# Performance work log

Measured on AMD Instinct MI355X. Metric: run time of the kernel, lower is better.

Reference implementation:

```python
import jax, jax.numpy as jnp
import numpy as np

B, T, H, NH, V = 2, 2048, 512, 8, 32000
HD = H // NH  # head dim

def setup_inputs() -> dict:
    key = jax.random.key(0)
    ks = jax.random.split(key, 15)
    s = 0.02
    rn = lambda k, shp: (jax.random.normal(k, shp, dtype=jnp.float32) * s)
    return {
        "ixs": jax.random.randint(ks[0], (B, T), 0, V, dtype=jnp.int32),
        "tok_emb": rn(ks[1], (V, H)),
        "pos_emb": rn(ks[2], (1, T, H)),
        "W_prj": rn(ks[3], (H, H)),
        "Wq": rn(ks[4], (H, H)), "bq": rn(ks[5], (H,)),
        "Wk": rn(ks[6], (H, H)), "bk": rn(ks[7], (H,)),
        "Wv": rn(ks[8], (H, H)), "bv": rn(ks[9], (H,)),
        "W1": rn(ks[10], (H, H)), "b1": rn(ks[11], (H,)),
        "W2": rn(ks[12], (V, H)), "b2": rn(ks[13], (V,)),
    }

def reference(ixs, tok_emb, pos_emb, W_prj, Wq, bq, Wk, bk, Wv, bv, W1, b1, W2, b2):
    b, t = ixs.shape
    # embeddings + projection (prj1 has no bias)
    x = tok_emb[ixs] + pos_emb[:, :t, :]          # [B,T,H]
    x = x @ W_prj.T                                # [B,T,H]
    # multi-head causal attention; NOTE: scale uses full hidden dim (allH**0.5)
    def heads(W, bias):
        return (x @ W.T + bias).reshape(b, t, NH, HD).transpose(0, 2, 1, 3)  # [B,nH,T,HD]
    q, k, v = heads(Wq, bq), heads(Wk, bk), heads(Wv, bv)
    att = jnp.einsum('bhqd,bhkd->bhqk', q, k) / (H ** 0.5)  # [B,nH,T,T]
    causal = jnp.tril(jnp.ones((t, t), dtype=bool))
    att = jnp.where(causal, att, -jnp.inf)
    w = jax.nn.softmax(att, axis=-1)
    y = jnp.einsum('bhqk,bhkd->bhqd', w, v)        # [B,nH,T,HD]
    y = y.transpose(0, 2, 1, 3).reshape(b, t, H)   # [B,T,H]
    # MLP: Linear->ReLU->Linear->ReLU (final ReLU per original loop condition)
    h1 = jax.nn.relu(y @ W1.T + b1)                # [B,T,H]
    out = jax.nn.relu(h1 @ W2.T + b2)              # [B,T,V]
    return out
```

## Files before the change

kernel.cpp:

```cpp
#include <hip/hip_runtime.h>
#include <stdint.h>
#include <stddef.h>

#define TSEQ   2048
#define HDIM   512
#define NHEADS 8
#define HEADD  64
#define NVOCAB 32000
#define NROWS  4096

typedef unsigned short ushort_t;
typedef __bf16 bf16x8 __attribute__((ext_vector_type(8)));
typedef float  f32x4  __attribute__((ext_vector_type(4)));
typedef unsigned short us8 __attribute__((ext_vector_type(8)));
typedef unsigned short us4 __attribute__((ext_vector_type(4)));
typedef unsigned short us2 __attribute__((ext_vector_type(2)));

__device__ __forceinline__ ushort_t f2bf(float f){
  union { float f; unsigned int u; } v; v.f = f;
  unsigned int u = v.u;
  u += 0x7FFFu + ((u >> 16) & 1u);
  return (ushort_t)(u >> 16);
}

__device__ __forceinline__ void gload_lds16(const ushort_t* g, ushort_t* l){
  __builtin_amdgcn_global_load_lds(
      (const __attribute__((address_space(1))) void*)g,
      (__attribute__((address_space(3))) void*)l, 16, 0, 0);
}

#define CVT_N4   4423680
#define CVT_TOT  4424064
__global__ void cvt_all_kernel(const float* __restrict__ Wprj, const float* __restrict__ Wq,
                               const float* __restrict__ Wk,   const float* __restrict__ Wv,
                               const float* __restrict__ W1,   const float* __restrict__ W2,
                               const float* __restrict__ bq,   const float* __restrict__ bk,
                               const float* __restrict__ bv,
                               ushort_t* __restrict__ wdst, float* __restrict__ bqkv){
  int stride = gridDim.x * blockDim.x;
  for (int i = blockIdx.x * blockDim.x + threadIdx.x; i < CVT_TOT; i += stride){
    if (i < CVT_N4){
      const float* src; int j;
      if (i < 327680){
        int w = i >> 16;
        j = i & 65535;
        src = (w == 0) ? Wprj : (w == 1) ? Wq : (w == 2) ? Wk : (w == 3) ? Wv : W1;
      } else {
        j = i - 327680;
        src = W2;
      }
      float4 f = ((const float4*)src)[j];
      us4 o;
      o[0] = f2bf(f.x); o[1] = f2bf(f.y); o[2] = f2bf(f.z); o[3] = f2bf(f.w);
      ((us4*)wdst)[i] = o;
    } else {
      int j = i - CVT_N4;
      const float* src = (j < 128) ? bq : (j < 256) ? bk : bv;
      int jj = j & 127;
      ((float4*)bqkv)[j] = ((const float4*)src)[jj];
    }
  }
}

__global__ void embed_kernel(const int* __restrict__ ixs, const float* __restrict__ tok,
                             const float* __restrict__ pos, ushort_t* __restrict__ x0){
  const int r = blockIdx.x;
  const int t = r & (TSEQ - 1);
  const int ix = ixs[r];
  const int j = threadIdx.x;
  const float2 a = ((const float2*)(tok + (size_t)ix * HDIM))[j];
  const float2 p = ((const float2*)(pos + (size_t)t * HDIM))[j];
  us2 o; o[0] = f2bf(a.x + p.x); o[1] = f2bf(a.y + p.y);
  *(us2*)(x0 + (size_t)r * HDIM + j * 2) = o;
}

template<int HAS_BIAS, int RELU, int OUT_F32>
__global__ __launch_bounds__(256) void gemm2_kernel(
    const ushort_t* __restrict__ A, const ushort_t* __restrict__ W,
    const float* __restrict__ bias, void* __restrict__ outp,
    int M, int N, int K)
{
  __shared__ ushort_t As[2][128 * 64];
  __shared__ ushort_t Bs[2][128 * 64];
  const int tid  = threadIdx.x;
  const int wave = tid >> 6;
  const int lane = tid & 63;
  const int lr   = lane & 15;
  const int lg   = lane >> 4;
  const int wr   = wave >> 1, wc = wave & 1;

  const int nwg = gridDim.x;
  const int cpx = nwg >> 3;
  const int g   = (blockIdx.x & 7) * cpx + (blockIdx.x >> 3);
  const int nby = M >> 7;
  const int by  = g % nby;
  const int bx  = g / nby;
  const int row0 = by << 7;
  const int col0 = bx << 7;

  f32x4 acc[4][4];
#pragma unroll
  for (int m = 0; m < 4; m++)
#pragma unroll
    for (int n = 0; n < 4; n++) acc[m][n] = (f32x4){0.f, 0.f, 0.f, 0.f};

  const int e    = tid * 8;
  const int srow = e >> 6;
  const int gch  = (((e & 63) >> 3) ^ (srow & 7)) * 8;
  const ushort_t* gA = A + (size_t)(row0 + srow) * K + gch;
  const ushort_t* gB = W + (size_t)(col0 + srow) * K + gch;
  const int ldsoff = wave * 512;

#pragma unroll
  for (int p = 0; p < 4; p++){
    gload_lds16(gA + (size_t)(p * 32) * K, &As[0][p * 2048 + ldsoff]);
    gload_lds16(gB + (size_t)(p * 32) * K, &Bs[0][p * 2048 + ldsoff]);
  }
  __syncthreads();

  const int NT = K >> 6;
  for (int t = 0; t < NT; ++t){
    const int cur = t & 1;
    if (t + 1 < NT){
      const int ko = (t + 1) << 6;
#pragma unroll
      for (int p = 0; p < 4; p++){
        gload_lds16(gA + (size_t)(p * 32) * K + ko, &As[cur ^ 1][p * 2048 + ldsoff]);
        gload_lds16(gB + (size_t)(p * 32) * K + ko, &Bs[cur ^ 1][p * 2048 + ldsoff]);
      }
    }
#pragma unroll
    for (int kk = 0; kk < 64; kk += 32){
      const int rch = (((kk >> 3) + lg) ^ (lr & 7)) * 8;
      bf16x8 af[4], bfr[4];
#pragma unroll
      for (int m = 0; m < 4; m++)
        af[m] = __builtin_bit_cast(bf16x8,
            *(const us8*)&As[cur][(wr * 64 + m * 16 + lr) * 64 + rch]);
#pragma unroll
      for (int n = 0; n < 4; n++)
        bfr[n] = __builtin_bit_cast(bf16x8,
            *(const us8*)&Bs[cur][(wc * 64 + n * 16 + lr) * 64 + rch]);
#pragma unroll
      for (int m = 0; m < 4; m++)
#pragma unroll
        for (int n = 0; n < 4; n++)
          acc[m][n] = __builtin_amdgcn_mfma_f32_16x16x32_bf16(bfr[n], af[m], acc[m][n], 0, 0, 0);
    }
    __syncthreads();
  }

#pragma unroll
  for (int n = 0; n < 4; n++){
    const int colb = col0 + wc * 64 + n * 16 + lg * 4;
    f32x4 b4 = (f32x4){0.f, 0.f, 0.f, 0.f};
    if (HAS_BIAS) b4 = *(const f32x4*)&bias[colb];
#pragma unroll
    for (int m = 0; m < 4; m++){
      const int row = row0 + wr * 64 + m * 16 + lr;
      float v0 = acc[m][n][0] + b4[0], v1 = acc[m][n][1] + b4[1];
      float v2 = acc[m][n][2] + b4[2], v3 = acc[m][n][3] + b4[3];
      if (RELU){ v0 = fmaxf(v0,0.f); v1 = fmaxf(v1,0.f); v2 = fmaxf(v2,0.f); v3 = fmaxf(v3,0.f); }
      if (OUT_F32){
        f32x4 o = {v0, v1, v2, v3};
        *(f32x4*)&((float*)outp)[(size_t)row * N + colb] = o;
      } else {
        us4 o; o[0] = f2bf(v0); o[1] = f2bf(v1); o[2] = f2bf(v2); o[3] = f2bf(v3);
        *(us4*)&((ushort_t*)outp)[(size_t)row * N + colb] = o;
      }
    }
  }
}

#define NKT 16
__global__ __launch_bounds__(512, 2) void gemm_big_kernel(
    const ushort_t* __restrict__ A, const ushort_t* __restrict__ W,
    const float* __restrict__ bias, float* __restrict__ outp)
{
  __shared__ ushort_t Asb[3][256 * 32];
  __shared__ ushort_t Bsb[3][256 * 32];
  const int K = HDIM, N = NVOCAB;
  const int tid  = threadIdx.x;
  const int wave = tid >> 6;
  const int lane = tid & 63;
  const int lr   = lane & 15;
  const int lg   = lane >> 4;
  const int wr   = wave >> 2;
  const int wc   = wave & 3;
  const int tt   = (blockIdx.x & 7) * 250 + (blockIdx.x >> 3);
  const int bx   = tt >> 4;
  const int by   = tt & 15;
  const int row0 = by << 8;
  const int col0 = bx << 8;

  const int rA   = tid >> 2;
  const int csw  = ((tid & 3) ^ (rA & 3) ^ ((rA >> 2) & 3)) * 8;
  const int swzc = (lg ^ (lr & 3) ^ ((lr >> 2) & 3)) * 8;

  f32x4 acc[8][4];
#pragma unroll
  for (int m = 0; m < 8; m++)
#pragma unroll
    for (int n = 0; n < 4; n++) acc[m][n] = (f32x4){0.f, 0.f, 0.f, 0.f};

  {
    const ushort_t* gA = A + (size_t)(row0 + rA) * K + csw;
    const ushort_t* gW = W + (size_t)(col0 + rA) * K + csw;
#pragma unroll
    for (int t = 0; t < 2; t++){
      gload_lds16(gA + t * 32,                       &Asb[t][wave * 512]);
      gload_lds16(gA + (size_t)128 * K + t * 32,     &Asb[t][4096 + wave * 512]);
      gload_lds16(gW + t * 32,                       &Bsb[t][wave * 512]);
      gload_lds16(gW + (size_t)128 * K + t * 32,     &Bsb[t][4096 + wave * 512]);
    }
  }
  asm volatile("s_waitcnt vmcnt(4)" ::: "memory");
  __builtin_amdgcn_s_barrier();

  for (int t = 0; t < NKT; ++t){
    const ushort_t* Ac = &Asb[t % 3][0];
    const ushort_t* Bc = &Bsb[t % 3][0];
    ushort_t* An = &Asb[(t + 2) % 3][0];
    ushort_t* Bn = &Bsb[(t + 2) % 3][0];
    const bool pf = (t + 2 < NKT);
    const int kg = (t + 2) * 32;

    bf16x8 bfr[4], af[4];
#pragma unroll
    for (int n = 0; n < 4; n++)
      bfr[n] = __builtin_bit_cast(bf16x8,
          *(const us8*)&Bc[(wc * 64 + n * 16 + lr) * 32 + swzc]);
#pragma unroll
    for (int q = 0; q < 4; q++)
      af[q] = __builtin_bit_cast(bf16x8,
          *(const us8*)&Ac[(wr * 128 + q * 16 + lr) * 32 + swzc]);
    if (pf){
      gload_lds16(A + (size_t)(row0 + rA) * K + kg + csw,       An + wave * 512);
      gload_lds16(A + (size_t)(row0 + rA + 128) * K + kg + csw, An + 4096 + wave * 512);
    }
    __builtin_amdgcn_s_barrier();
    asm volatile("s_waitcnt lgkmcnt(0)" ::: "memory");
    __builtin_amdgcn_sched_barrier(0);
    __builtin_amdgcn_s_setprio(1);
#pragma unroll
    for (int q = 0; q < 4; q++)
#pragma unroll
      for (int n = 0; n < 4; n++)
        acc[q][n] = __builtin_amdgcn_mfma_f32_16x16x32_bf16(bfr[n], af[q], acc[q][n], 0, 0, 0);
    __builtin_amdgcn_s_setprio(0);
    __builtin_amdgcn_sched_barrier(0);
    __builtin_amdgcn_s_barrier();

#pragma unroll
    for (int q = 0; q < 4; q++)
      af[q] = __builtin_bit_cast(bf16x8,
          *(const us8*)&Ac[(wr * 128 + (q + 4) * 16 + lr) * 32 + swzc]);
    if (pf){
      gload_lds16(W + (size_t)(col0 + rA) * K + kg + csw,       Bn + wave * 512);
      gload_lds16(W + (size_t)(col0 + rA + 128) * K + kg + csw, Bn + 4096 + wave * 512);
    }
    __builtin_amdgcn_s_barrier();
    asm volatile("s_waitcnt lgkmcnt(0)" ::: "memory");
    __builtin_amdgcn_sched_barrier(0);
    __builtin_amdgcn_s_setprio(1);
#pragma unroll
    for (int q = 0; q < 4; q++)
#pragma unroll
      for (int n = 0; n < 4; n++)
        acc[q + 4][n] = __builtin_amdgcn_mfma_f32_16x16x32_bf16(bfr[n], af[q], acc[q + 4][n], 0, 0, 0);
    __builtin_amdgcn_s_setprio(0);
    __builtin_amdgcn_sched_barrier(0);
    if (t < NKT - 2) { asm volatile("s_waitcnt vmcnt(4)" ::: "memory"); }
    else             { asm volatile("s_waitcnt vmcnt(0)" ::: "memory"); }
    __builtin_amdgcn_s_barrier();
  }

#pragma unroll
  for (int n = 0; n < 4; n++){
    const int colb = col0 + wc * 64 + n * 16 + lg * 4;
    const f32x4 b4 = *(const f32x4*)&bias[colb];
#pragma unroll
    for (int m = 0; m < 8; m++){
      const int row = row0 + wr * 128 + m * 16 + lr;
      f32x4 o;
      o[0] = fmaxf(acc[m][n][0] + b4[0], 0.f);
      o[1] = fmaxf(acc[m][n][1] + b4[1], 0.f);
      o[2] = fmaxf(acc[m][n][2] + b4[2], 0.f);
      o[3] = fmaxf(acc[m][n][3] + b4[3], 0.f);
      __builtin_nontemporal_store(o, (f32x4*)&outp[(size_t)row * N + colb]);
    }
  }
}

__global__ __launch_bounds__(256) void attn_kernel(
    const ushort_t* __restrict__ qkv, ushort_t* __restrict__ y)
{
  __shared__ ushort_t Ks[64 * 64];
  __shared__ ushort_t Vt[64 * 64];
  __shared__ ushort_t Ps[4][16 * 64];
  const int qt   = 31 - blockIdx.x;
  const int hb   = blockIdx.y;
  const int b    = hb >> 3;
  const int h    = hb & 7;
  const int tid  = threadIdx.x;
  const int wave = tid >> 6, lane = tid & 63;
  const int lr   = lane & 15, lg = lane >> 4;
  const int ld   = 3 * HDIM;
  const size_t rowbase = (size_t)b * TSEQ;
  const ushort_t* kb = qkv + HDIM;
  const ushort_t* vb = qkv + 2 * HDIM;

  const int qrow = qt * 64 + wave * 16 + lr;
  const ushort_t* qp = qkv + (rowbase + qrow) * ld + h * HEADD;
  bf16x8 qf[2];
  qf[0] = __builtin_bit_cast(bf16x8, *(const us8*)&qp[lg * 8]);
  qf[1] = __builtin_bit_cast(bf16x8, *(const us8*)&qp[32 + lg * 8]);

  float m_run[4], l_run[4];
  f32x4 acc_o[4];
#pragma unroll
  for (int i = 0; i < 4; i++){ m_run[i] = -1e30f; l_run[i] = 0.f; acc_o[i] = (f32x4){0,0,0,0}; }

  const int e    = tid * 8;
  const int srow = e >> 6;
  const int scol = e & 63;
  const float scale = 0.04419417382415922f;

  for (int kt = 0; kt <= qt; ++kt){
    const ushort_t* gK = kb + (rowbase + kt * 64 + srow) * ld + h * HEADD + scol;
    gload_lds16(gK,                     &Ks[wave * 512]);
    gload_lds16(gK + (size_t)32 * ld,   &Ks[2048 + wave * 512]);
    const ushort_t* gV = vb + (rowbase + kt * 64 + srow) * ld + h * HEADD + scol;
    us8 v0 = *(const us8*)gV;
    us8 v1 = *(const us8*)(gV + (size_t)32 * ld);
#pragma unroll
    for (int j = 0; j < 8; j++){
      Vt[(scol + j) * 64 + srow]      = v0[j];
      Vt[(scol + j) * 64 + srow + 32] = v1[j];
    }
    __syncthreads();

    f32x4 s[4];
#pragma unroll
    for (int n = 0; n < 4; n++){
      s[n] = (f32x4){0, 0, 0, 0};
#pragma unroll
      for (int ks = 0; ks < 2; ks++){
        bf16x8 kf = __builtin_bit_cast(bf16x8,
            *(const us8*)&Ks[(n * 16 + lr) * 64 + ks * 32 + lg * 8]);
        s[n] = __builtin_amdgcn_mfma_f32_16x16x32_bf16(qf[ks], kf, s[n], 0, 0, 0);
      }
    }

    float sv[4][4];
    float tmax[4] = {-1e30f, -1e30f, -1e30f, -1e30f};
    const bool diag = (kt == qt);
#pragma unroll
    for (int n = 0; n < 4; n++)
#pragma unroll
      for (int r = 0; r < 4; r++){
        float x = s[n][r] * scale;
        if (diag && (n * 16 + lr) > (wave * 16 + lg * 4 + r)) x = -1e30f;
        sv[n][r] = x;
        tmax[r] = fmaxf(tmax[r], x);
      }
#pragma unroll
    for (int off = 1; off < 16; off <<= 1)
#pragma unroll
      for (int r = 0; r < 4; r++) tmax[r] = fmaxf(tmax[r], __shfl_xor(tmax[r], off));

    float alpha[4], psum[4];
#pragma unroll
    for (int r = 0; r < 4; r++){
      float mn = fmaxf(m_run[r], tmax[r]);
      alpha[r] = __expf(m_run[r] - mn);
      m_run[r] = mn;
      psum[r] = 0.f;
    }
    float p[4][4];
#pragma unroll
    for (int n = 0; n < 4; n++)
#pragma unroll
      for (int r = 0; r < 4; r++){ p[n][r] = __expf(sv[n][r] - m_run[r]); psum[r] += p[n][r]; }
#pragma unroll
    for (int off = 1; off < 16; off <<= 1)
#pragma unroll
      for (int r = 0; r < 4; r++) psum[r] += __shfl_xor(psum[r], off);
#pragma unroll
    for (int r = 0; r < 4; r++) l_run[r] = l_run[r] * alpha[r] + psum[r];
#pragma unroll
    for (int nd = 0; nd < 4; nd++)
#pragma unroll
      for (int r = 0; r < 4; r++) acc_o[nd][r] *= alpha[r];

#pragma unroll
    for (int n = 0; n < 4; n++)
#pragma unroll
      for (int r = 0; r < 4; r++)
        Ps[wave][(lg * 4 + r) * 64 + n * 16 + lr] = f2bf(p[n][r]);
    asm volatile("s_waitcnt lgkmcnt(0)" ::: "memory");
    bf16x8 pa[2];
    pa[0] = __builtin_bit_cast(bf16x8, *(const us8*)&Ps[wave][lr * 64 + lg * 8]);
    pa[1] = __builtin_bit_cast(bf16x8, *(const us8*)&Ps[wave][lr * 64 + 32 + lg * 8]);
#pragma unroll
    for (int nd = 0; nd < 4; nd++)
#pragma unroll
      for (int ks = 0; ks < 2; ks++){
        bf16x8 vf = __builtin_bit_cast(bf16x8,
            *(const us8*)&Vt[(nd * 16 + lr) * 64 + ks * 32 + lg * 8]);
        acc_o[nd] = __builtin_amdgcn_mfma_f32_16x16x32_bf16(pa[ks], vf, acc_o[nd], 0, 0, 0);
      }
    __syncthreads();
  }

  float inv[4];
#pragma unroll
  for (int r = 0; r < 4; r++) inv[r] = 1.f / l_run[r];
#pragma unroll
  for (int nd = 0; nd < 4; nd++)
#pragma unroll
    for (int r = 0; r < 4; r++){
      const int row_t = qt * 64 + wave * 16 + lg * 4 + r;
      y[(rowbase + row_t) * HDIM + h * HEADD + nd * 16 + lr] = f2bf(acc_o[nd][r] * inv[r]);
    }
}

extern "C" void kernel_launch(void* const* d_in, const int* in_sizes, int n_in,
                              void* d_out, int out_size, void* d_ws, size_t ws_size,
                              hipStream_t stream)
{
  const int*   ixs  = (const int*)  d_in[0];
  const float* tok  = (const float*)d_in[1];
  const float* pos  = (const float*)d_in[2];
  const float* Wprj = (const float*)d_in[3];
  const float* Wq   = (const float*)d_in[4];
  const float* bq_  = (const float*)d_in[5];
  const float* Wk   = (const float*)d_in[6];
  const float* bk_  = (const float*)d_in[7];
  const float* Wv   = (const float*)d_in[8];
  const float* bv_  = (const float*)d_in[9];
  const float* W1   = (const float*)d_in[10];
  const float* b1_  = (const float*)d_in[11];
  const float* W2   = (const float*)d_in[12];
  const float* b2_  = (const float*)d_in[13];
  float* out = (float*)d_out;

  ushort_t* ws    = (ushort_t*)d_ws;
  ushort_t* x0    = ws;
  ushort_t* x1    = x0    + 2097152;
  ushort_t* qkv   = x1    + 2097152;
  ushort_t* yb    = qkv   + 6291456;
  ushort_t* h1b   = yb    + 2097152;
  ushort_t* wprjb = h1b   + 2097152;
  ushort_t* wqkvb = wprjb + 262144;
  ushort_t* w1b   = wqkvb + 786432;
  ushort_t* w2b   = w1b   + 262144;
  float*    bqkv  = (float*)(w2b + 16384000);

  cvt_all_kernel<<<2048, 256, 0, stream>>>(Wprj, Wq, Wk, Wv, W1, W2,
                                           bq_, bk_, bv_, wprjb, bqkv);

  embed_kernel<<<NROWS, 256, 0, stream>>>(ixs, tok, pos, x0);

  gemm2_kernel<0,0,0><<<32 * 4,   256, 0, stream>>>(x0,  wprjb, nullptr, x1,  NROWS, 512,   512);
  gemm2_kernel<1,0,0><<<32 * 12,  256, 0, stream>>>(x1,  wqkvb, bqkv,    qkv, NROWS, 1536,  512);
  attn_kernel<<<dim3(32, 16), 256, 0, stream>>>(qkv, yb);
  gemm2_kernel<1,1,0><<<32 * 4,   256, 0, stream>>>(yb,  w1b,   b1_,     h1b, NROWS, 512,   512);
  gemm_big_kernel<<<2000, 512, 0, stream>>>(h1b, w2b, b2_, out);
}
```

Before: 421.5 us.

## Restructure vocab GEMM pipeline to double-buffered BK=64 with four-phase interleaved loads

The large output GEMM moves from a triple-buffered K-tile of 32 with two phases per iteration to a double-buffered K-tile of 64 split into four phases. Each phase issues a slice of next-tile global-to-LDS loads. The change also uses a new 8-way XOR swizzle, drops the blockIdx remapping for L2 locality, relaxes launch bounds to one block per SM, and switches nontemporal stores to plain stores. The aim is fewer barriers per K step and more MFMA work per phase. The cost is lower occupancy and a different cache footprint.

New measurement: 464.6 us. +10.2%, slower.

```diff
diff --git a/kernel.cpp b/kernel.cpp
--- a/kernel.cpp
+++ b/kernel.cpp
@@ -172,13 +172,13 @@
   }
 }
 
-#define NKT 16
-__global__ __launch_bounds__(512, 2) void gemm_big_kernel(
+#define VNT2 8
+__global__ __launch_bounds__(512, 1) void gemm_big_kernel(
     const ushort_t* __restrict__ A, const ushort_t* __restrict__ W,
     const float* __restrict__ bias, float* __restrict__ outp)
 {
-  __shared__ ushort_t Asb[3][256 * 32];
-  __shared__ ushort_t Bsb[3][256 * 32];
+  __shared__ ushort_t As[2][256 * 64];
+  __shared__ ushort_t Bs[2][256 * 64];
   const int K = HDIM, N = NVOCAB;
   const int tid  = threadIdx.x;
   const int wave = tid >> 6;
@@ -187,15 +187,16 @@
   const int lg   = lane >> 4;
   const int wr   = wave >> 2;
   const int wc   = wave & 3;
-  const int tt   = (blockIdx.x & 7) * 250 + (blockIdx.x >> 3);
-  const int bx   = tt >> 4;
-  const int by   = tt & 15;
+  const int by   = blockIdx.x & 15;
+  const int bx   = blockIdx.x >> 4;
   const int row0 = by << 8;
   const int col0 = bx << 8;
 
-  const int rA   = tid >> 2;
-  const int csw  = ((tid & 3) ^ (rA & 3) ^ ((rA >> 2) & 3)) * 8;
-  const int swzc = (lg ^ (lr & 3) ^ ((lr >> 2) & 3)) * 8;
+  const int srow8 = tid >> 3;
+  const int gch   = (((tid & 7) ^ (srow8 & 7))) * 8;
+  const int ldsoff = wave * 512;
+  const ushort_t* gA = A + (size_t)(row0 + srow8) * K + gch;
+  const ushort_t* gW = W + (size_t)(col0 + srow8) * K + gch;
 
   f32x4 acc[8][4];
 #pragma unroll
@@ -203,76 +204,85 @@
 #pragma unroll
     for (int n = 0; n < 4; n++) acc[m][n] = (f32x4){0.f, 0.f, 0.f, 0.f};
 
-  {
-    const ushort_t* gA = A + (size_t)(row0 + rA) * K + csw;
-    const ushort_t* gW = W + (size_t)(col0 + rA) * K + csw;
-#pragma unroll
-    for (int t = 0; t < 2; t++){
-      gload_lds16(gA + t * 32,                       &Asb[t][wave * 512]);
-      gload_lds16(gA + (size_t)128 * K + t * 32,     &Asb[t][4096 + wave * 512]);
-      gload_lds16(gW + t * 32,                       &Bsb[t][wave * 512]);
-      gload_lds16(gW + (size_t)128 * K + t * 32,     &Bsb[t][4096 + wave * 512]);
-    }
-  }
-  asm volatile("s_waitcnt vmcnt(4)" ::: "memory");
+#pragma unroll
+  for (int p = 0; p < 4; p++)
+    gload_lds16(gW + (size_t)(p * 64) * K, &Bs[0][p * 4096 + ldsoff]);
+  gload_lds16(gA,                      &As[0][0 * 4096 + ldsoff]);
+  gload_lds16(gA + (size_t)128 * K,    &As[0][2 * 4096 + ldsoff]);
+  gload_lds16(gA + (size_t)64 * K,     &As[0][1 * 4096 + ldsoff]);
+  gload_lds16(gA + (size_t)192 * K,    &As[0][3 * 4096 + ldsoff]);
+  asm volatile("s_waitcnt vmcnt(0)" ::: "memory");
   __builtin_amdgcn_s_barrier();
 
-  for (int t = 0; t < NKT; ++t){
-    const ushort_t* Ac = &Asb[t % 3][0];
-    const ushort_t* Bc = &Bsb[t % 3][0];
-    ushort_t* An = &Asb[(t + 2) % 3][0];
-    ushort_t* Bn = &Bsb[(t + 2) % 3][0];
-    const bool pf = (t + 2 < NKT);
-    const int kg = (t + 2) * 32;
-
-    bf16x8 bfr[4], af[4];
-#pragma unroll
-    for (int n = 0; n < 4; n++)
-      bfr[n] = __builtin_bit_cast(bf16x8,
-          *(const us8*)&Bc[(wc * 64 + n * 16 + lr) * 32 + swzc]);
-#pragma unroll
-    for (int q = 0; q < 4; q++)
-      af[q] = __builtin_bit_cast(bf16x8,
-          *(const us8*)&Ac[(wr * 128 + q * 16 + lr) * 32 + swzc]);
-    if (pf){
-      gload_lds16(A + (size_t)(row0 + rA) * K + kg + csw,       An + wave * 512);
-      gload_lds16(A + (size_t)(row0 + rA + 128) * K + kg + csw, An + 4096 + wave * 512);
-    }
-    __builtin_amdgcn_s_barrier();
-    asm volatile("s_waitcnt lgkmcnt(0)" ::: "memory");
-    __builtin_amdgcn_sched_barrier(0);
-    __builtin_amdgcn_s_setprio(1);
-#pragma unroll
-    for (int q = 0; q < 4; q++)
-#pragma unroll
-      for (int n = 0; n < 4; n++)
-        acc[q][n] = __builtin_amdgcn_mfma_f32_16x16x32_bf16(bfr[n], af[q], acc[q][n], 0, 0, 0);
-    __builtin_amdgcn_s_setprio(0);
-    __builtin_amdgcn_sched_barrier(0);
-    __builtin_amdgcn_s_barrier();
-
-#pragma unroll
-    for (int q = 0; q < 4; q++)
-      af[q] = __builtin_bit_cast(bf16x8,
-          *(const us8*)&Ac[(wr * 128 + (q + 4) * 16 + lr) * 32 + swzc]);
-    if (pf){
-      gload_lds16(W + (size_t)(col0 + rA) * K + kg + csw,       Bn + wave * 512);
-      gload_lds16(W + (size_t)(col0 + rA + 128) * K + kg + csw, Bn + 4096 + wave * 512);
-    }
-    __builtin_amdgcn_s_barrier();
-    asm volatile("s_waitcnt lgkmcnt(0)" ::: "memory");
-    __builtin_amdgcn_sched_barrier(0);
-    __builtin_amdgcn_s_setprio(1);
-#pragma unroll
-    for (int q = 0; q < 4; q++)
-#pragma unroll
-      for (int n = 0; n < 4; n++)
-        acc[q + 4][n] = __builtin_amdgcn_mfma_f32_16x16x32_bf16(bfr[n], af[q], acc[q + 4][n], 0, 0, 0);
-    __builtin_amdgcn_s_setprio(0);
-    __builtin_amdgcn_sched_barrier(0);
-    if (t < NKT - 2) { asm volatile("s_waitcnt vmcnt(4)" ::: "memory"); }
-    else             { asm volatile("s_waitcnt vmcnt(0)" ::: "memory"); }
-    __builtin_amdgcn_s_barrier();
+  bf16x8 bfr[4][2];
+  for (int t = 0; t < VNT2; ++t){
+    const int cur = t & 1;
+    const ushort_t* Ac = &As[cur][0];
+    const ushort_t* Bc = &Bs[cur][0];
+    ushort_t* An = &As[cur ^ 1][0];
+    ushort_t* Bn = &Bs[cur ^ 1][0];
+    const bool pf = (t + 1 < VNT2);
+    const int kg = (t + 1) << 6;
+
+#pragma unroll
+    for (int p = 0; p < 4; ++p){
+      bf16x8 af[2][2];
+#pragma unroll
+      for (int mm = 0; mm < 2; mm++){
+        const int R = wr * 128 + (2 * p + mm) * 16 + lr;
+#pragma unroll
+        for (int k2 = 0; k2 < 2; k2++){
+          const int pos = ((k2 * 4 + lg) ^ (lr & 7)) * 8;
+          af[mm][k2] = __builtin_bit_cast(bf16x8, *(const us8*)&Ac[R * 64 + pos]);
+        }
+      }
+      if (p == 0){
+#pragma unroll
+        for (int n = 0; n < 4; n++){
+          const int R = wc * 64 + n * 16 + lr;
+#pragma unroll
+          for (int k2 = 0; k2 < 2; k2++){
+            const int pos = ((k2 * 4 + lg) ^ (lr & 7)) * 8;
+            bfr[n][k2] = __builtin_bit_cast(bf16x8, *(const us8*)&Bc[R * 64 + pos]);
+          }
+        }
+      }
+      if (pf){
+        if (p == 0){
+          gload_lds16(gW + (size_t)(0 * 64) * K + kg, &Bn[0 * 4096 + ldsoff]);
+          gload_lds16(gW + (size_t)(1 * 64) * K + kg, &Bn[1 * 4096 + ldsoff]);
+        } else if (p == 1){
+          gload_lds16(gW + (size_t)(2 * 64) * K + kg, &Bn[2 * 4096 + ldsoff]);
+          gload_lds16(gW + (size_t)(3 * 64) * K + kg, &Bn[3 * 4096 + ldsoff]);
+        } else if (p == 2){
+          gload_lds16(gA + kg,                   &An[0 * 4096 + ldsoff]);
+          gload_lds16(gA + (size_t)128 * K + kg, &An[2 * 4096 + ldsoff]);
+        } else {
+          gload_lds16(gA + (size_t)64 * K + kg,  &An[1 * 4096 + ldsoff]);
+          gload_lds16(gA + (size_t)192 * K + kg, &An[3 * 4096 + ldsoff]);
+        }
+      }
+      __builtin_amdgcn_s_barrier();
+      asm volatile("s_waitcnt lgkmcnt(0)" ::: "memory");
+      __builtin_amdgcn_sched_barrier(0);
+      __builtin_amdgcn_s_setprio(1);
+#pragma unroll
+      for (int mm = 0; mm < 2; mm++)
+#pragma unroll
+        for (int n = 0; n < 4; n++)
+#pragma unroll
+          for (int k2 = 0; k2 < 2; k2++)
+            acc[2 * p + mm][n] = __builtin_amdgcn_mfma_f32_16x16x32_bf16(
+                bfr[n][k2], af[mm][k2], acc[2 * p + mm][n], 0, 0, 0);
+      __builtin_amdgcn_s_setprio(0);
+      __builtin_amdgcn_sched_barrier(0);
+      if (p == 1){ asm volatile("s_waitcnt vmcnt(4)" ::: "memory"); }
+      if (p == 3){
+        if (pf) { asm volatile("s_waitcnt vmcnt(2)" ::: "memory"); }
+        else    { asm volatile("s_waitcnt vmcnt(0)" ::: "memory"); }
+      }
+      __builtin_amdgcn_s_barrier();
+    }
   }
 
 #pragma unroll
@@ -287,7 +297,7 @@
       o[1] = fmaxf(acc[m][n][1] + b4[1], 0.f);
       o[2] = fmaxf(acc[m][n][2] + b4[2], 0.f);
       o[3] = fmaxf(acc[m][n][3] + b4[3], 0.f);
-      __builtin_nontemporal_store(o, (f32x4*)&outp[(size_t)row * N + colb]);
+      *(f32x4*)&outp[(size_t)row * N + colb] = o;
     }
   }
 }
```
